# Kernel optimization log

Hardware: AMD Instinct MI355X
Metric: run time of the kernel (lower is better)

## Reference

```python
import jax, jax.numpy as jnp
import numpy as np

B, T, D, H = 2, 2048, 1024, 16
DH = D // H


def setup_inputs() -> dict:
    key = jax.random.key(0)
    ks = jax.random.split(key, 8)
    s = 1.0 / np.sqrt(D)  # xavier-ish scale
    return {
        "query": jax.random.normal(ks[0], (B, T, D), jnp.float32),
        "key": jax.random.normal(ks[1], (B, T, D), jnp.float32),
        "value": jax.random.normal(ks[2], (B, T, D), jnp.float32),
        "Wq": jax.random.normal(ks[3], (D, D), jnp.float32) * s,
        "bq": jnp.zeros((D,), jnp.float32),
        "Wk": jax.random.normal(ks[4], (D, D), jnp.float32) * s,
        "bk": jnp.zeros((D,), jnp.float32),
        "Wv": jax.random.normal(ks[5], (D, D), jnp.float32) * s,
        "bv": jnp.zeros((D,), jnp.float32),
        "Wo": jax.random.normal(ks[6], (D, D), jnp.float32) * s,
        "bo": jnp.zeros((D,), jnp.float32),
        # causal mask (B, T, T); True = attend
        "mask": jnp.broadcast_to(jnp.tril(jnp.ones((T, T), bool)), (B, T, T)),
    }


def _split_heads(x):  # (B, T, D) -> (B, H, T, Dh)
    return x.reshape(B, T, H, DH).transpose(0, 2, 1, 3)


def reference(query, key, value, Wq, bq, Wk, bk, Wv, bv, Wo, bo, mask):
    q = _split_heads(query @ Wq + bq)
    k = _split_heads(key @ Wk + bk)
    v = _split_heads(value @ Wv + bv)
    scores = jnp.einsum("bhqd,bhkd->bhqk", q, k) / jnp.sqrt(jnp.float32(DH))
    scores = jnp.where(mask[:, None, :, :], scores, -jnp.inf)
    w = jax.nn.softmax(scores, axis=-1)
    out = jnp.einsum("bhqk,bhkd->bhqd", w, v)
    out = out.transpose(0, 2, 1, 3).reshape(B, T, D)  # merge heads
    return out @ Wo + bo
```

## Files before the change

kernel.cpp:

```cpp
#include <hip/hip_runtime.h>

typedef unsigned short u16;
typedef __attribute__((ext_vector_type(4))) float f32x4;
typedef __attribute__((ext_vector_type(8))) short bf16x8;

#define MFMA16(a,b,c) __builtin_amdgcn_mfma_f32_16x16x32_bf16((a),(b),(c),0,0,0)

__device__ inline u16 f2bf(float f){
  union { float f; unsigned u; } v; v.f = f;
  unsigned r = v.u + 0x7FFFu + ((v.u >> 16) & 1u);
  return (u16)(r >> 16);
}
__device__ inline u16 f2bf_fast(float f){
  union { float f; unsigned u; } v; v.f = f;
  return (u16)((v.u + 0x8000u) >> 16);
}

typedef const __attribute__((address_space(1))) unsigned int* gas_ptr;
typedef __attribute__((address_space(3))) unsigned int* las_ptr;
__device__ inline void gload_lds16(const u16* g, u16* l){
  __builtin_amdgcn_global_load_lds((gas_ptr)(const void*)g, (las_ptr)(void*)l, 16, 0, 0);
}

template<int N>
__device__ inline float rorf(float v){
  union { float f; int i; } a, b; a.f = v;
  b.i = __builtin_amdgcn_update_dpp(a.i, a.i, 0x120|N, 0xF, 0xF, false);
  return b.f;
}
__device__ inline float redMax16(float v){
  v = fmaxf(v, rorf<8>(v)); v = fmaxf(v, rorf<4>(v));
  v = fmaxf(v, rorf<2>(v)); v = fmaxf(v, rorf<1>(v));
  return v;
}

struct CvtArgs { const float* x[3]; u16* y[3]; };
__global__ void k_cvt3(CvtArgs a, int n4){
  const float* x = a.x[blockIdx.y];
  u16* y = a.y[blockIdx.y];
  int i = blockIdx.x*blockDim.x + threadIdx.x;
  if (i < n4){
    float4 v = ((const float4*)x)[i];
    ushort4 o;
    o.x = f2bf(v.x); o.y = f2bf(v.y); o.z = f2bf(v.z); o.w = f2bf(v.w);
    ((ushort4*)y)[i] = o;
  }
}

struct TwbArgs { const float* W[4]; u16* Wt[4]; };
__global__ void k_twb4(TwbArgs a){
  __shared__ u16 t[32][33];
  const float* W = a.W[blockIdx.z];
  u16* Wt = a.Wt[blockIdx.z];
  int kb = blockIdx.x*32, nb = blockIdx.y*32;
  int tx = threadIdx.x, ty = threadIdx.y;
  #pragma unroll
  for (int i=0;i<32;i+=8)
    t[ty+i][tx] = f2bf(W[(size_t)(kb+ty+i)*1024 + nb+tx]);
  __syncthreads();
  #pragma unroll
  for (int i=0;i<32;i+=8)
    Wt[(size_t)(nb+ty+i)*1024 + kb+tx] = t[tx][ty+i];
}

__global__ void k_tv(const u16* __restrict__ V, u16* __restrict__ VT){
  __shared__ u16 t[32][33];
  int tb = blockIdx.x*32;
  int db = blockIdx.y*32;
  int bh = blockIdx.z;
  int b = bh>>4, h = bh&15;
  int tx = threadIdx.x, ty = threadIdx.y;
  #pragma unroll
  for (int i=0;i<32;i+=8)
    t[ty+i][tx] = V[(size_t)(b*2048 + tb+ty+i)*1024 + h*64 + db+tx];
  __syncthreads();
  #pragma unroll
  for (int i=0;i<32;i+=8)
    VT[(size_t)(bh*64 + db+ty+i)*2048 + tb+tx] = t[tx][ty+i];
}

struct GemmArgs3 { const u16* A[3]; const u16* Bt[3]; const float* bias[3]; u16* C[3]; };
__global__ __launch_bounds__(256) void k_gemm3(GemmArgs3 g){
  const int N=1024, K=1024;
  int flat = blockIdx.x + (blockIdx.y<<5) + (blockIdx.z<<8);
  int swz = (flat&7)*96 + (flat>>3);
  int by = swz & 7, bx = (swz>>3) & 31, bz = swz >> 8;
  const u16* A = g.A[bz]; const u16* Bt = g.Bt[bz];
  const float* bias = g.bias[bz]; u16* C = g.C[bz];
  __shared__ __attribute__((aligned(16))) u16 As[128*64];
  __shared__ __attribute__((aligned(16))) u16 Bs[128*64];
  const int tid  = threadIdx.x;
  const int wave = tid>>6, lane = tid&63;
  const int lo = lane&15, hi = lane>>4;
  const int row0 = bx*128, col0 = by*128;
  const int wm = (wave>>1)*64, wn = (wave&1)*64;
  f32x4 acc[4][4];
  #pragma unroll
  for (int i=0;i<4;i++)
    #pragma unroll
    for (int j=0;j<4;j++) acc[i][j] = (f32x4){0.f,0.f,0.f,0.f};

  for (int k0=0; k0<K; k0+=64){
    #pragma unroll
    for (int r=0;r<4;r++){
      int c = r*256 + tid;
      gload_lds16(A  + (size_t)(row0 + (c>>3))*K + k0 + (c&7)*8, As + c*8);
      gload_lds16(Bt + (size_t)(col0 + (c>>3))*K + k0 + (c&7)*8, Bs + c*8);
    }
    __syncthreads();
    __builtin_amdgcn_s_setprio(1);
    #pragma unroll
    for (int ks=0;ks<2;ks++){
      bf16x8 af[4], bfr[4];
      #pragma unroll
      for (int mf=0;mf<4;mf++)
        af[mf] = *(const bf16x8*)(As + (wm+mf*16+lo)*64 + ks*32 + hi*8);
      #pragma unroll
      for (int nf=0;nf<4;nf++)
        bfr[nf] = *(const bf16x8*)(Bs + (wn+nf*16+lo)*64 + ks*32 + hi*8);
      #pragma unroll
      for (int mf=0;mf<4;mf++)
        #pragma unroll
        for (int nf=0;nf<4;nf++)
          acc[mf][nf] = MFMA16(af[mf], bfr[nf], acc[mf][nf]);
    }
    __builtin_amdgcn_s_setprio(0);
    __syncthreads();
  }
  #pragma unroll
  for (int mf=0;mf<4;mf++){
    #pragma unroll
    for (int nf=0;nf<4;nf++){
      int r0 = row0 + wm + mf*16 + hi*4;
      int c0 = col0 + wn + nf*16 + lo;
      float bv = bias[c0];
      #pragma unroll
      for (int r=0;r<4;r++)
        C[(size_t)(r0+r)*N + c0] = f2bf(acc[mf][nf][r] + bv);
    }
  }
}

__global__ __launch_bounds__(256) void k_gemmO(const u16* __restrict__ A, const u16* __restrict__ Bt,
                                               const float* __restrict__ bias, float* __restrict__ C){
  const int N=1024, K=1024;
  int f = blockIdx.x;
  int xcd = f & 7, idx = f >> 3;
  int bx = xcd*8 + (idx>>3), by = idx & 7;
  __shared__ __attribute__((aligned(16))) u16 As[64*64];
  __shared__ __attribute__((aligned(16))) u16 Bs[128*64];
  const int tid  = threadIdx.x;
  const int wave = tid>>6, lane = tid&63;
  const int lo = lane&15, hi = lane>>4;
  const int row0 = bx*64, col0 = by*128;
  const int wm = (wave>>1)*32, wn = (wave&1)*64;
  f32x4 acc[2][4];
  #pragma unroll
  for (int i=0;i<2;i++)
    #pragma unroll
    for (int j=0;j<4;j++) acc[i][j] = (f32x4){0.f,0.f,0.f,0.f};

  for (int k0=0; k0<K; k0+=64){
    #pragma unroll
    for (int r=0;r<2;r++){
      int c = r*256 + tid;
      gload_lds16(A + (size_t)(row0 + (c>>3))*K + k0 + (c&7)*8, As + c*8);
    }
    #pragma unroll
    for (int r=0;r<4;r++){
      int c = r*256 + tid;
      gload_lds16(Bt + (size_t)(col0 + (c>>3))*K + k0 + (c&7)*8, Bs + c*8);
    }
    __syncthreads();
    __builtin_amdgcn_s_setprio(1);
    #pragma unroll
    for (int ks=0;ks<2;ks++){
      bf16x8 af[2], bfr[4];
      #pragma unroll
      for (int mf=0;mf<2;mf++)
        af[mf] = *(const bf16x8*)(As + (wm+mf*16+lo)*64 + ks*32 + hi*8);
      #pragma unroll
      for (int nf=0;nf<4;nf++)
        bfr[nf] = *(const bf16x8*)(Bs + (wn+nf*16+lo)*64 + ks*32 + hi*8);
      #pragma unroll
      for (int mf=0;mf<2;mf++)
        #pragma unroll
        for (int nf=0;nf<4;nf++)
          acc[mf][nf] = MFMA16(af[mf], bfr[nf], acc[mf][nf]);
    }
    __builtin_amdgcn_s_setprio(0);
    __syncthreads();
  }
  #pragma unroll
  for (int mf=0;mf<2;mf++){
    #pragma unroll
    for (int nf=0;nf<4;nf++){
      int r0 = row0 + wm + mf*16 + hi*4;
      int c0 = col0 + wn + nf*16 + lo;
      float bv = bias[c0];
      #pragma unroll
      for (int r=0;r<4;r++)
        C[(size_t)(r0+r)*N + c0] = acc[mf][nf][r] + bv;
    }
  }
}

__global__ __launch_bounds__(256) void k_attn(
    const u16* __restrict__ Q, const u16* __restrict__ Kp,
    const u16* __restrict__ VT, u16* __restrict__ O)
{
  const int T=2048, D=1024;
  __shared__ __attribute__((aligned(16))) u16 Ks[2][64*64];
  __shared__ __attribute__((aligned(16))) u16 Vs[2][64*64];
  __shared__ __attribute__((aligned(16))) u16 Plds[4][16*64];
  int f = blockIdx.x + (blockIdx.y<<5);
  int xcd = f & 7, idx = f >> 3;
  const int bh = (xcd<<2) | (idx&3);
  const int qb = 31 - (idx>>2);
  const int b = bh>>4, h = bh&15;
  const int tid = threadIdx.x;
  const int wave = tid>>6, lane = tid&63;
  const int lo = lane&15, hi = lane>>4;
  const float NEG = -__builtin_inff();
  const float sc = 0.125f * 1.44269504f;
  const bf16x8 ones = {0x3F80,0x3F80,0x3F80,0x3F80,0x3F80,0x3F80,0x3F80,0x3F80};

  const int cof0 = ((hi    ) ^ (lo&7))*8;
  const int cof1 = ((hi + 4) ^ (lo&7))*8;

  const int c0 = tid, c1 = 256 + tid;
  const int sr0 = c0>>3, sj0 = (c0&7)^(sr0&7);
  const int sr1 = c1>>3, sj1 = (c1&7)^(sr1&7);
  const u16* Kbase = Kp + (size_t)(b*T)*D + h*64;
  const u16* Vbase = VT + (size_t)(bh*64)*T;
  const size_t kOff0 = (size_t)sr0*D + sj0*8, kOff1 = (size_t)sr1*D + sj1*8;
  const size_t vOff0 = (size_t)sr0*T + sj0*8, vOff1 = (size_t)sr1*T + sj1*8;

  const int qrow0 = qb*64 + wave*16;
  const u16* Qb = Q + (size_t)(b*T + qrow0 + lo)*D + h*64;
  bf16x8 qf0 = *(const bf16x8*)(Qb + hi*8);
  bf16x8 qf1 = *(const bf16x8*)(Qb + 32 + hi*8);

  f32x4 o[4];
  #pragma unroll
  for (int nf=0;nf<4;nf++) o[nf] = (f32x4){0.f,0.f,0.f,0.f};
  float m[4], l[4];
  #pragma unroll
  for (int r=0;r<4;r++){ m[r] = NEG; l[r] = 0.f; }

  gload_lds16(Kbase + kOff0, &Ks[0][c0*8]);
  gload_lds16(Kbase + kOff1, &Ks[0][c1*8]);
  gload_lds16(Vbase + vOff0, &Vs[0][c0*8]);
  gload_lds16(Vbase + vOff1, &Vs[0][c1*8]);
  __syncthreads();

  int cur = 0;
  for (int kb=0; kb<=qb; kb++){
    if (kb < qb){
      const u16* Kt = Kbase + (size_t)(kb+1)*64*D;
      const u16* Vt = Vbase + (kb+1)*64;
      gload_lds16(Kt + kOff0, &Ks[cur^1][c0*8]);
      gload_lds16(Kt + kOff1, &Ks[cur^1][c1*8]);
      gload_lds16(Vt + vOff0, &Vs[cur^1][c0*8]);
      gload_lds16(Vt + vOff1, &Vs[cur^1][c1*8]);
    }
    const u16* Kl = Ks[cur];
    const u16* Vl = Vs[cur];
    f32x4 s[4];
    __builtin_amdgcn_s_setprio(1);
    #pragma unroll
    for (int nf=0;nf<4;nf++){
      int row = nf*16 + lo;
      bf16x8 kf0 = *(const bf16x8*)(Kl + row*64 + cof0);
      bf16x8 kf1 = *(const bf16x8*)(Kl + row*64 + cof1);
      f32x4 z = (f32x4){0.f,0.f,0.f,0.f};
      z = MFMA16(qf0, kf0, z);
      s[nf] = MFMA16(qf1, kf1, z);
    }
    __builtin_amdgcn_s_setprio(0);
    float pm[4] = {NEG,NEG,NEG,NEG};
    if (kb == qb){
      #pragma unroll
      for (int nf=0;nf<4;nf++){
        int col = kb*64 + nf*16 + lo;
        #pragma unroll
        for (int r=0;r<4;r++){
          int row = qrow0 + hi*4 + r;
          if (col > row) s[nf][r] = NEG;
          pm[r] = fmaxf(pm[r], s[nf][r]);
        }
      }
    } else {
      #pragma unroll
      for (int nf=0;nf<4;nf++)
        #pragma unroll
        for (int r=0;r<4;r++)
          pm[r] = fmaxf(pm[r], s[nf][r]);
    }
    #pragma unroll
    for (int r=0;r<4;r++) pm[r] = redMax16(pm[r]);
    bool small = true;
    #pragma unroll
    for (int r=0;r<4;r++) small = small && (pm[r] <= m[r] + 44.f);
    const bool resc = !__all(small);
    float alpha[4];
    if (resc){
      #pragma unroll
      for (int r=0;r<4;r++){
        float mn = fmaxf(m[r], pm[r]);
        alpha[r] = __builtin_amdgcn_exp2f((m[r] - mn)*sc);
        m[r] = mn;
      }
      #pragma unroll
      for (int nf=0;nf<4;nf++)
        #pragma unroll
        for (int r=0;r<4;r++) o[nf][r] *= alpha[r];
    }
    float msc[4];
    #pragma unroll
    for (int r=0;r<4;r++) msc[r] = m[r]*sc;
    #pragma unroll
    for (int nf=0;nf<4;nf++)
      #pragma unroll
      for (int r=0;r<4;r++){
        float p = __builtin_amdgcn_exp2f(__builtin_fmaf(s[nf][r], sc, -msc[r]));
        int prow = hi*4+r, pcol = nf*16+lo;
        Plds[wave][prow*64 + (pcol ^ ((prow&7)<<3))] = f2bf_fast(p);
      }
    bf16x8 pa0 = *(const bf16x8*)(&Plds[wave][lo*64 + cof0]);
    bf16x8 pa1 = *(const bf16x8*)(&Plds[wave][lo*64 + cof1]);
    f32x4 lsum = (f32x4){0.f,0.f,0.f,0.f};
    __builtin_amdgcn_s_setprio(1);
    lsum = MFMA16(pa0, ones, lsum);
    lsum = MFMA16(pa1, ones, lsum);
    #pragma unroll
    for (int nf=0;nf<4;nf++){
      int row = nf*16 + lo;
      bf16x8 v0 = *(const bf16x8*)(Vl + row*64 + cof0);
      bf16x8 v1 = *(const bf16x8*)(Vl + row*64 + cof1);
      o[nf] = MFMA16(pa0, v0, o[nf]);
      o[nf] = MFMA16(pa1, v1, o[nf]);
    }
    __builtin_amdgcn_s_setprio(0);
    if (resc){
      #pragma unroll
      for (int r=0;r<4;r++) l[r] = l[r]*alpha[r] + lsum[r];
    } else {
      #pragma unroll
      for (int r=0;r<4;r++) l[r] += lsum[r];
    }
    __syncthreads();
    cur ^= 1;
  }
  #pragma unroll
  for (int nf=0;nf<4;nf++)
    #pragma unroll
    for (int r=0;r<4;r++){
      int row = qrow0 + hi*4 + r;
      O[(size_t)(b*T+row)*D + h*64 + nf*16 + lo] = f2bf_fast(o[nf][r] / l[r]);
    }
}

extern "C" void kernel_launch(void* const* d_in, const int* in_sizes, int n_in,
                              void* d_out, int out_size, void* d_ws, size_t ws_size,
                              hipStream_t stream) {
  const int B=2, T=2048, D=1024;
  const int M = B*T;
  const float* query = (const float*)d_in[0];
  const float* key   = (const float*)d_in[1];
  const float* value = (const float*)d_in[2];
  const float* Wq = (const float*)d_in[3];  const float* bq = (const float*)d_in[4];
  const float* Wk = (const float*)d_in[5];  const float* bk = (const float*)d_in[6];
  const float* Wv = (const float*)d_in[7];  const float* bv = (const float*)d_in[8];
  const float* Wo = (const float*)d_in[9];  const float* bo = (const float*)d_in[10];
  float* out = (float*)d_out;

  char* ws = (char*)d_ws;
  const size_t MB = 1024*1024;
  u16* xq  = (u16*)(ws + 0*MB);
  u16* xk  = (u16*)(ws + 8*MB);
  u16* xv  = (u16*)(ws + 16*MB);
  u16* WqT = (u16*)(ws + 24*MB);
  u16* WkT = (u16*)(ws + 26*MB);
  u16* WvT = (u16*)(ws + 28*MB);
  u16* WoT = (u16*)(ws + 30*MB);
  u16* Qp  = (u16*)(ws + 32*MB);
  u16* Kp  = (u16*)(ws + 40*MB);
  u16* Vp  = (u16*)(ws + 48*MB);
  u16* VTp = (u16*)(ws + 56*MB);
  u16* AO  = (u16*)(ws + 64*MB);

  int n4 = M*D/4;
  CvtArgs ca; ca.x[0]=query; ca.x[1]=key; ca.x[2]=value; ca.y[0]=xq; ca.y[1]=xk; ca.y[2]=xv;
  k_cvt3<<<dim3(n4/256, 3), 256, 0, stream>>>(ca, n4);

  TwbArgs ta; ta.W[0]=Wq; ta.W[1]=Wk; ta.W[2]=Wv; ta.W[3]=Wo;
  ta.Wt[0]=WqT; ta.Wt[1]=WkT; ta.Wt[2]=WvT; ta.Wt[3]=WoT;
  k_twb4<<<dim3(32,32,4), dim3(32,8), 0, stream>>>(ta);

  GemmArgs3 ga;
  ga.A[0]=xq; ga.A[1]=xk; ga.A[2]=xv;
  ga.Bt[0]=WqT; ga.Bt[1]=WkT; ga.Bt[2]=WvT;
  ga.bias[0]=bq; ga.bias[1]=bk; ga.bias[2]=bv;
  ga.C[0]=Qp; ga.C[1]=Kp; ga.C[2]=Vp;
  k_gemm3<<<dim3(32,8,3), 256, 0, stream>>>(ga);

  k_tv<<<dim3(T/32, 2, 32), dim3(32,8), 0, stream>>>(Vp, VTp);
  k_attn<<<dim3(32,32), 256, 0, stream>>>(Qp, Kp, VTp, AO);
  k_gemmO<<<512, 256, 0, stream>>>(AO, WoT, bo, out);
}
```

Before: 129.5 us.

## Rewrite attention with 32x32 MFMA, 128-row query tiles, and register-resident P

The attention kernel now uses 32x32x16 MFMAs with each wave owning 32 query rows, so a block covers 128 query rows and each K/V tile loaded into LDS is reused by twice as many queries. Scores are computed transposed (K as the A operand), so each lane owns a single query row: the row max and sum need only one cross-half shuffle, and P is repacked into the B operand in registers with shuffles instead of a round trip through LDS. Waves whose diagonal block comes earlier skip compute for the last K block, and the grid is halved. The costs are higher register pressure from 16-wide accumulators and fewer blocks to fill the device.

```diff
diff --git a/kernel.cpp b/kernel.cpp
--- a/kernel.cpp
+++ b/kernel.cpp
@@ -2,9 +2,11 @@
 
 typedef unsigned short u16;
 typedef __attribute__((ext_vector_type(4))) float f32x4;
+typedef __attribute__((ext_vector_type(16))) float f32x16;
 typedef __attribute__((ext_vector_type(8))) short bf16x8;
 
 #define MFMA16(a,b,c) __builtin_amdgcn_mfma_f32_16x16x32_bf16((a),(b),(c),0,0,0)
+#define MFMA32(a,b,c) __builtin_amdgcn_mfma_f32_32x32x16_bf16((a),(b),(c),0,0,0)
 
 __device__ inline u16 f2bf(float f){
   union { float f; unsigned u; } v; v.f = f;
@@ -20,18 +22,6 @@
 typedef __attribute__((address_space(3))) unsigned int* las_ptr;
 __device__ inline void gload_lds16(const u16* g, u16* l){
   __builtin_amdgcn_global_load_lds((gas_ptr)(const void*)g, (las_ptr)(void*)l, 16, 0, 0);
-}
-
-template<int N>
-__device__ inline float rorf(float v){
-  union { float f; int i; } a, b; a.f = v;
-  b.i = __builtin_amdgcn_update_dpp(a.i, a.i, 0x120|N, 0xF, 0xF, false);
-  return b.f;
-}
-__device__ inline float redMax16(float v){
-  v = fmaxf(v, rorf<8>(v)); v = fmaxf(v, rorf<4>(v));
-  v = fmaxf(v, rorf<2>(v)); v = fmaxf(v, rorf<1>(v));
-  return v;
 }
 
 struct CvtArgs { const float* x[3]; u16* y[3]; };
@@ -212,21 +202,27 @@
   const int T=2048, D=1024;
   __shared__ __attribute__((aligned(16))) u16 Ks[2][64*64];
   __shared__ __attribute__((aligned(16))) u16 Vs[2][64*64];
-  __shared__ __attribute__((aligned(16))) u16 Plds[4][16*64];
-  int f = blockIdx.x + (blockIdx.y<<5);
+  int f = blockIdx.x;
   int xcd = f & 7, idx = f >> 3;
   const int bh = (xcd<<2) | (idx&3);
-  const int qb = 31 - (idx>>2);
+  const int qq = 15 - (idx>>2);
   const int b = bh>>4, h = bh&15;
   const int tid = threadIdx.x;
   const int wave = tid>>6, lane = tid&63;
-  const int lo = lane&15, hi = lane>>4;
+  const int la = lane&31, hi5 = lane>>5;
   const float NEG = -__builtin_inff();
   const float sc = 0.125f * 1.44269504f;
-  const bf16x8 ones = {0x3F80,0x3F80,0x3F80,0x3F80,0x3F80,0x3F80,0x3F80,0x3F80};
-
-  const int cof0 = ((hi    ) ^ (lo&7))*8;
-  const int cof1 = ((hi + 4) ^ (lo&7))*8;
+
+  const int kbmax = 2*qq + 1;
+  const int kb_d  = 2*qq + (wave>>1);
+
+  const int la7 = la & 7;
+  int cofK[4], cofV[4];
+  #pragma unroll
+  for (int i=0;i<4;i++){
+    cofK[i] = ((2*i + hi5) ^ la7)*8;
+    cofV[i] = ((2*i + hi5) ^ la7)*8;
+  }
 
   const int c0 = tid, c1 = 256 + tid;
   const int sr0 = c0>>3, sj0 = (c0&7)^(sr0&7);
@@ -236,17 +232,20 @@
   const size_t kOff0 = (size_t)sr0*D + sj0*8, kOff1 = (size_t)sr1*D + sj1*8;
   const size_t vOff0 = (size_t)sr0*T + sj0*8, vOff1 = (size_t)sr1*T + sj1*8;
 
-  const int qrow0 = qb*64 + wave*16;
-  const u16* Qb = Q + (size_t)(b*T + qrow0 + lo)*D + h*64;
-  bf16x8 qf0 = *(const bf16x8*)(Qb + hi*8);
-  bf16x8 qf1 = *(const bf16x8*)(Qb + 32 + hi*8);
-
-  f32x4 o[4];
-  #pragma unroll
-  for (int nf=0;nf<4;nf++) o[nf] = (f32x4){0.f,0.f,0.f,0.f};
-  float m[4], l[4];
-  #pragma unroll
-  for (int r=0;r<4;r++){ m[r] = NEG; l[r] = 0.f; }
+  const int qrow0 = qq*128 + wave*32;
+  const int qglob = qrow0 + la;
+  const u16* Qrow = Q + (size_t)(b*T + qglob)*D + h*64;
+  bf16x8 qf[4];
+  #pragma unroll
+  for (int dq=0;dq<4;dq++)
+    qf[dq] = *(const bf16x8*)(Qrow + dq*16 + hi5*8);
+
+  f32x16 o2[2];
+  #pragma unroll
+  for (int i=0;i<2;i++)
+    #pragma unroll
+    for (int r=0;r<16;r++) o2[i][r] = 0.f;
+  float m = NEG, l = 0.f;
 
   gload_lds16(Kbase + kOff0, &Ks[0][c0*8]);
   gload_lds16(Kbase + kOff1, &Ks[0][c1*8]);
@@ -255,8 +254,8 @@
   __syncthreads();
 
   int cur = 0;
-  for (int kb=0; kb<=qb; kb++){
-    if (kb < qb){
+  for (int kb=0; kb<=kbmax; kb++){
+    if (kb < kbmax){
       const u16* Kt = Kbase + (size_t)(kb+1)*64*D;
       const u16* Vt = Vbase + (kb+1)*64;
       gload_lds16(Kt + kOff0, &Ks[cur^1][c0*8]);
@@ -264,100 +263,115 @@
       gload_lds16(Vt + vOff0, &Vs[cur^1][c0*8]);
       gload_lds16(Vt + vOff1, &Vs[cur^1][c1*8]);
     }
-    const u16* Kl = Ks[cur];
-    const u16* Vl = Vs[cur];
-    f32x4 s[4];
-    __builtin_amdgcn_s_setprio(1);
-    #pragma unroll
-    for (int nf=0;nf<4;nf++){
-      int row = nf*16 + lo;
-      bf16x8 kf0 = *(const bf16x8*)(Kl + row*64 + cof0);
-      bf16x8 kf1 = *(const bf16x8*)(Kl + row*64 + cof1);
-      f32x4 z = (f32x4){0.f,0.f,0.f,0.f};
-      z = MFMA16(qf0, kf0, z);
-      s[nf] = MFMA16(qf1, kf1, z);
-    }
-    __builtin_amdgcn_s_setprio(0);
-    float pm[4] = {NEG,NEG,NEG,NEG};
-    if (kb == qb){
-      #pragma unroll
-      for (int nf=0;nf<4;nf++){
-        int col = kb*64 + nf*16 + lo;
-        #pragma unroll
-        for (int r=0;r<4;r++){
-          int row = qrow0 + hi*4 + r;
-          if (col > row) s[nf][r] = NEG;
-          pm[r] = fmaxf(pm[r], s[nf][r]);
+    if (kb <= kb_d){
+      const u16* Kl = Ks[cur];
+      const u16* Vl = Vs[cur];
+      f32x16 s2[2];
+      __builtin_amdgcn_s_setprio(1);
+      #pragma unroll
+      for (int kt=0;kt<2;kt++){
+        f32x16 acc;
+        #pragma unroll
+        for (int r=0;r<16;r++) acc[r] = 0.f;
+        #pragma unroll
+        for (int dq=0;dq<4;dq++){
+          bf16x8 kf = *(const bf16x8*)(Kl + (kt*32+la)*64 + cofK[dq]);
+          acc = MFMA32(kf, qf[dq], acc);
         }
+        s2[kt] = acc;
       }
-    } else {
-      #pragma unroll
-      for (int nf=0;nf<4;nf++)
-        #pragma unroll
-        for (int r=0;r<4;r++)
-          pm[r] = fmaxf(pm[r], s[nf][r]);
-    }
-    #pragma unroll
-    for (int r=0;r<4;r++) pm[r] = redMax16(pm[r]);
-    bool small = true;
-    #pragma unroll
-    for (int r=0;r<4;r++) small = small && (pm[r] <= m[r] + 44.f);
-    const bool resc = !__all(small);
-    float alpha[4];
-    if (resc){
-      #pragma unroll
-      for (int r=0;r<4;r++){
-        float mn = fmaxf(m[r], pm[r]);
-        alpha[r] = __builtin_amdgcn_exp2f((m[r] - mn)*sc);
-        m[r] = mn;
+      __builtin_amdgcn_s_setprio(0);
+      bf16x8 vf[2][4];
+      #pragma unroll
+      for (int dht=0;dht<2;dht++)
+        #pragma unroll
+        for (int kc=0;kc<4;kc++)
+          vf[dht][kc] = *(const bf16x8*)(Vl + (dht*32+la)*64 + cofV[kc]);
+      if (kb == kb_d){
+        int kbase = kb*64 + 4*hi5;
+        #pragma unroll
+        for (int kt=0;kt<2;kt++)
+          #pragma unroll
+          for (int r=0;r<16;r++){
+            int kg = kbase + kt*32 + (r&3) + 8*(r>>2);
+            if (kg > qglob) s2[kt][r] = NEG;
+          }
       }
-      #pragma unroll
-      for (int nf=0;nf<4;nf++)
-        #pragma unroll
-        for (int r=0;r<4;r++) o[nf][r] *= alpha[r];
-    }
-    float msc[4];
-    #pragma unroll
-    for (int r=0;r<4;r++) msc[r] = m[r]*sc;
-    #pragma unroll
-    for (int nf=0;nf<4;nf++)
-      #pragma unroll
-      for (int r=0;r<4;r++){
-        float p = __builtin_amdgcn_exp2f(__builtin_fmaf(s[nf][r], sc, -msc[r]));
-        int prow = hi*4+r, pcol = nf*16+lo;
-        Plds[wave][prow*64 + (pcol ^ ((prow&7)<<3))] = f2bf_fast(p);
+      float pm = s2[0][0];
+      #pragma unroll
+      for (int r=1;r<16;r++) pm = fmaxf(pm, s2[0][r]);
+      #pragma unroll
+      for (int r=0;r<16;r++) pm = fmaxf(pm, s2[1][r]);
+      pm = fmaxf(pm, __shfl_xor(pm, 32));
+      const bool resc = !__all(pm <= m + 44.f);
+      float alpha = 1.f;
+      if (resc){
+        float mn = fmaxf(m, pm);
+        alpha = __builtin_amdgcn_exp2f((m - mn)*sc);
+        m = mn;
+        #pragma unroll
+        for (int i=0;i<2;i++)
+          #pragma unroll
+          for (int r=0;r<16;r++) o2[i][r] *= alpha;
       }
-    bf16x8 pa0 = *(const bf16x8*)(&Plds[wave][lo*64 + cof0]);
-    bf16x8 pa1 = *(const bf16x8*)(&Plds[wave][lo*64 + cof1]);
-    f32x4 lsum = (f32x4){0.f,0.f,0.f,0.f};
-    __builtin_amdgcn_s_setprio(1);
-    lsum = MFMA16(pa0, ones, lsum);
-    lsum = MFMA16(pa1, ones, lsum);
-    #pragma unroll
-    for (int nf=0;nf<4;nf++){
-      int row = nf*16 + lo;
-      bf16x8 v0 = *(const bf16x8*)(Vl + row*64 + cof0);
-      bf16x8 v1 = *(const bf16x8*)(Vl + row*64 + cof1);
-      o[nf] = MFMA16(pa0, v0, o[nf]);
-      o[nf] = MFMA16(pa1, v1, o[nf]);
-    }
-    __builtin_amdgcn_s_setprio(0);
-    if (resc){
-      #pragma unroll
-      for (int r=0;r<4;r++) l[r] = l[r]*alpha[r] + lsum[r];
-    } else {
-      #pragma unroll
-      for (int r=0;r<4;r++) l[r] += lsum[r];
+      const float msc = m*sc;
+      float ls = 0.f;
+      unsigned w[2][8];
+      #pragma unroll
+      for (int kt=0;kt<2;kt++)
+        #pragma unroll
+        for (int e=0;e<8;e++){
+          float p0 = __builtin_amdgcn_exp2f(__builtin_fmaf(s2[kt][2*e],   sc, -msc));
+          float p1 = __builtin_amdgcn_exp2f(__builtin_fmaf(s2[kt][2*e+1], sc, -msc));
+          ls += p0 + p1;
+          union { float f; unsigned u; } ua, ub; ua.f = p0; ub.f = p1;
+          w[kt][e] = ((ua.u + 0x8000u) >> 16) | ((ub.u + 0x8000u) & 0xFFFF0000u);
+        }
+      ls += __shfl_xor(ls, 32);
+      l = resc ? (l*alpha + ls) : (l + ls);
+      unsigned pw[2][8];
+      #pragma unroll
+      for (int kt=0;kt<2;kt++)
+        #pragma unroll
+        for (int e=0;e<8;e++) pw[kt][e] = __shfl_xor(w[kt][e], 32);
+      union { unsigned u[4]; bf16x8 v; } pbu[4];
+      #pragma unroll
+      for (int kt=0;kt<2;kt++){
+        pbu[2*kt  ].u[0] = hi5 ? pw[kt][2] : w[kt][0];
+        pbu[2*kt  ].u[1] = hi5 ? pw[kt][3] : w[kt][1];
+        pbu[2*kt  ].u[2] = hi5 ? w[kt][2]  : pw[kt][0];
+        pbu[2*kt  ].u[3] = hi5 ? w[kt][3]  : pw[kt][1];
+        pbu[2*kt+1].u[0] = hi5 ? pw[kt][6] : w[kt][4];
+        pbu[2*kt+1].u[1] = hi5 ? pw[kt][7] : w[kt][5];
+        pbu[2*kt+1].u[2] = hi5 ? w[kt][6]  : pw[kt][4];
+        pbu[2*kt+1].u[3] = hi5 ? w[kt][7]  : pw[kt][5];
+      }
+      __builtin_amdgcn_s_setprio(1);
+      #pragma unroll
+      for (int dht=0;dht<2;dht++){
+        f32x16 acc = o2[dht];
+        #pragma unroll
+        for (int kc=0;kc<4;kc++)
+          acc = MFMA32(vf[dht][kc], pbu[kc].v, acc);
+        o2[dht] = acc;
+      }
+      __builtin_amdgcn_s_setprio(0);
     }
     __syncthreads();
     cur ^= 1;
   }
-  #pragma unroll
-  for (int nf=0;nf<4;nf++)
-    #pragma unroll
-    for (int r=0;r<4;r++){
-      int row = qrow0 + hi*4 + r;
-      O[(size_t)(b*T+row)*D + h*64 + nf*16 + lo] = f2bf_fast(o[nf][r] / l[r]);
+  float rl = 1.f / l;
+  u16* Orow = O + (size_t)(b*T + qglob)*D + h*64;
+  #pragma unroll
+  for (int dht=0;dht<2;dht++)
+    #pragma unroll
+    for (int rr=0;rr<4;rr++){
+      ushort4 pk;
+      pk.x = f2bf_fast(o2[dht][rr*4+0]*rl);
+      pk.y = f2bf_fast(o2[dht][rr*4+1]*rl);
+      pk.z = f2bf_fast(o2[dht][rr*4+2]*rl);
+      pk.w = f2bf_fast(o2[dht][rr*4+3]*rl);
+      *(ushort4*)(Orow + dht*32 + rr*8 + hi5*4) = pk;
     }
 }
 
@@ -406,6 +420,6 @@
   k_gemm3<<<dim3(32,8,3), 256, 0, stream>>>(ga);
 
   k_tv<<<dim3(T/32, 2, 32), dim3(32,8), 0, stream>>>(Vp, VTp);
-  k_attn<<<dim3(32,32), 256, 0, stream>>>(Qp, Kp, VTp, AO);
+  k_attn<<<512, 256, 0, stream>>>(Qp, Kp, VTp, AO);
   k_gemmO<<<512, 256, 0, stream>>>(AO, WoT, bo, out);
 }
```

New measurement: 136.3 us. 1.05x slower.
